# Performance work log

Measured on AMD Instinct MI355X. Metric: run time of the kernel, lower is better.

The kernel has to match this reference:

```python
import jax, jax.numpy as jnp
import numpy as np

H = 16  # num_heads (inner_dim 1024 // default head_dim 64)
D = 64  # head_dim
EPS = 1e-5

def layernorm(x, w, b):
    mu = jnp.mean(x, axis=-1, keepdims=True)
    var = jnp.var(x, axis=-1, keepdims=True)
    return (x - mu) * jax.lax.rsqrt(var + EPS) * w + b

def attention(x, kv, wq, wk, wv, wo, bo):
    b, t, c = x.shape
    s = kv.shape[1]
    q = (x @ wq).reshape(b, t, H, D).transpose(0, 2, 1, 3)   # bhtd
    k = (kv @ wk).reshape(b, s, H, D).transpose(0, 2, 1, 3)  # bhsd
    v = (kv @ wv).reshape(b, s, H, D).transpose(0, 2, 1, 3)
    scores = jnp.einsum('bhqd,bhkd->bhqk', q, k) * (D ** -0.5)
    attn = jax.nn.softmax(scores, axis=-1)
    out = jnp.einsum('bhqk,bhkd->bhqd', attn, v)
    out = out.transpose(0, 2, 1, 3).reshape(b, t, c)
    return out @ wo + bo

def setup_inputs() -> dict:
    key = jax.random.key(0)
    ks = jax.random.split(key, 16)
    hs = 1024
    dff = 4 * hs  # 4096
    sc = lambda fan_in: 1.0 / np.sqrt(fan_in)
    inp = {
        'x': jax.random.normal(ks[0], (2, 2048, hs), jnp.float32),
        'encoder_hidden_states': jax.random.normal(ks[1], (2, 512, 64), jnp.float32),
        'ln1_w': jnp.ones((hs,), jnp.float32), 'ln1_b': jnp.zeros((hs,), jnp.float32),
        'a1_wq': jax.random.normal(ks[2], (hs, hs), jnp.float32) * sc(hs),
        'a1_wk': jax.random.normal(ks[3], (hs, hs), jnp.float32) * sc(hs),
        'a1_wv': jax.random.normal(ks[4], (hs, hs), jnp.float32) * sc(hs),
        'a1_wo': jax.random.normal(ks[5], (hs, hs), jnp.float32) * sc(hs),
        'a1_bo': jnp.zeros((hs,), jnp.float32),
        'ln2_w': jnp.ones((hs,), jnp.float32), 'ln2_b': jnp.zeros((hs,), jnp.float32),
        'a2_wq': jax.random.normal(ks[6], (hs, hs), jnp.float32) * sc(hs),
        'a2_wk': jax.random.normal(ks[7], (64, hs), jnp.float32) * sc(64),
        'a2_wv': jax.random.normal(ks[8], (64, hs), jnp.float32) * sc(64),
        'a2_wo': jax.random.normal(ks[9], (hs, hs), jnp.float32) * sc(hs),
        'a2_bo': jnp.zeros((hs,), jnp.float32),
        'ln3_w': jnp.ones((hs,), jnp.float32), 'ln3_b': jnp.zeros((hs,), jnp.float32),
        'ff_w1': jax.random.normal(ks[10], (hs, 2 * dff), jnp.float32) * sc(hs),
        'ff_b1': jnp.zeros((2 * dff,), jnp.float32),
        'ff_w2': jax.random.normal(ks[11], (dff, hs), jnp.float32) * sc(dff),
        'ff_b2': jnp.zeros((hs,), jnp.float32),
    }
    return inp

def reference(x, encoder_hidden_states, ln1_w, ln1_b, a1_wq, a1_wk, a1_wv, a1_wo, a1_bo,
              ln2_w, ln2_b, a2_wq, a2_wk, a2_wv, a2_wo, a2_bo,
              ln3_w, ln3_b, ff_w1, ff_b1, ff_w2, ff_b2):
    # self-attention sub-block
    h = layernorm(x, ln1_w, ln1_b)
    x = x + attention(h, h, a1_wq, a1_wk, a1_wv, a1_wo, a1_bo)
    # cross-attention sub-block (kv from encoder_hidden_states, dim 64)
    h = layernorm(x, ln2_w, ln2_b)
    x = x + attention(h, encoder_hidden_states, a2_wq, a2_wk, a2_wv, a2_wo, a2_bo)
    # GEGLU feed-forward sub-block
    h = layernorm(x, ln3_w, ln3_b)
    hp = h @ ff_w1 + ff_b1
    h1, h2 = jnp.split(hp, 2, axis=-1)
    h = (h1 * jax.nn.gelu(h2, approximate=False)) @ ff_w2 + ff_b2
    return x + h
```

## Files before the change

### kernel.cpp

```cpp
#include <hip/hip_runtime.h>
#include <hip/hip_bf16.h>
#include <stdint.h>

typedef unsigned short u16;
typedef __bf16 bf16x8 __attribute__((ext_vector_type(8)));
typedef float f32x4 __attribute__((ext_vector_type(4)));
typedef u16 u16x8 __attribute__((ext_vector_type(8)));
typedef u16 u16x4 __attribute__((ext_vector_type(4)));

__device__ __forceinline__ u16 f2bf(float f) {
  union { float f; uint32_t u; } v; v.f = f;
  uint32_t r = v.u + 0x7fffu + ((v.u >> 16) & 1u);
  return (u16)(r >> 16);
}
__device__ __forceinline__ float bf2f(u16 u) {
  union { uint32_t u; float f; } v; v.u = ((uint32_t)u) << 16;
  return v.f;
}
__device__ __forceinline__ uint32_t cvtpk(float a, float b) {
  uint32_t r;
  asm("v_cvt_pk_bf16_f32 %0, %1, %2" : "=v"(r) : "v"(a), "v"(b));
  return r;
}

__device__ __forceinline__ void gld16(const u16* g, u16* l) {
  __builtin_amdgcn_global_load_lds(
      (const __attribute__((address_space(1))) uint32_t*)g,
      (__attribute__((address_space(3))) uint32_t*)l, 16, 0, 0);
}

__device__ __forceinline__ void stage_half(const u16* __restrict__ gbase, int ldg,
                                           u16* lbase, int tid) {
#pragma unroll
  for (int j = 0; j < 2; ++j) {
    const int idx = j * 512 + tid;
    const int row = idx >> 3, c8 = idx & 7;
    gld16(gbase + (size_t)row * ldg + ((c8 ^ (row & 7)) << 3), lbase + idx * 8);
  }
}

struct WB {
  const float* src[6];
  u16* dst[6];
  float scale[6];
};
__global__ void wconv_b(WB wb, int K, int N) {
  const int z = blockIdx.z;
  const float* __restrict__ W = wb.src[z];
  u16* __restrict__ Wt = wb.dst[z];
  const float scale = wb.scale[z];
  __shared__ float tile[32][33];
  const int n0 = blockIdx.x * 32, k0 = blockIdx.y * 32;
  const int tx = threadIdx.x, ty = threadIdx.y;
#pragma unroll
  for (int i = 0; i < 4; ++i)
    tile[ty + 8 * i][tx] = W[(size_t)(k0 + ty + 8 * i) * N + n0 + tx];
  __syncthreads();
#pragma unroll
  for (int i = 0; i < 4; ++i)
    Wt[(size_t)(n0 + ty + 8 * i) * K + k0 + tx] = f2bf(scale * tile[tx][ty + 8 * i]);
}

__global__ void wconv_t(const float* __restrict__ W, u16* __restrict__ Wt, int K, int N) {
  __shared__ float tile[32][33];
  const int n0 = blockIdx.x * 32, k0 = blockIdx.y * 32;
  const int tx = threadIdx.x, ty = threadIdx.y;
#pragma unroll
  for (int i = 0; i < 4; ++i)
    tile[ty + 8 * i][tx] = W[(size_t)(k0 + ty + 8 * i) * N + n0 + tx];
  __syncthreads();
#pragma unroll
  for (int i = 0; i < 4; ++i)
    Wt[(size_t)(n0 + ty + 8 * i) * K + k0 + tx] = f2bf(tile[tx][ty + 8 * i]);
}

__global__ void wconv_g(const float* __restrict__ W, u16* __restrict__ Wt) {
  __shared__ float tile[32][33];
  const int n0 = blockIdx.x * 32, k0 = blockIdx.y * 32;
  const int tx = threadIdx.x, ty = threadIdx.y;
#pragma unroll
  for (int i = 0; i < 4; ++i)
    tile[ty + 8 * i][tx] = W[(size_t)(k0 + ty + 8 * i) * 8192 + n0 + tx];
  __syncthreads();
#pragma unroll
  for (int i = 0; i < 4; ++i) {
    const int n = n0 + ty + 8 * i;
    const int p = (((n & 4095) >> 7) << 8) + (((n >> 12) & 1) << 7) + (n & 127);
    Wt[(size_t)p * 1024 + k0 + tx] = f2bf(tile[tx][ty + 8 * i]);
  }
}

__global__ void cvt_bf(const float* __restrict__ in, u16* __restrict__ out, int n) {
  int i = blockIdx.x * 256 + threadIdx.x;
  if (i < n) out[i] = f2bf(in[i]);
}

__global__ __launch_bounds__(256)
void vtrans(const u16* __restrict__ V, int ldv, int hoff, u16* __restrict__ Vt, int S) {
  __shared__ u16 tile[64][72];
  const int t0 = blockIdx.x, bh = blockIdx.y;
  const int b = bh >> 4, hc = (bh & 15) * 64 + hoff;
  const int tid = threadIdx.x;
  const int r = tid >> 2, dq = (tid & 3) * 16;
  const int pos = ((r >> 5) << 5) | (((r >> 2) & 3) << 3) | (((r >> 4) & 1) << 2) | (r & 3);
  const size_t grow = ((size_t)b * S + t0 * 64 + r) * ldv + hc + dq;
  u16x8 v1 = *(const u16x8*)&V[grow];
  u16x8 v2 = *(const u16x8*)&V[grow + 8];
#pragma unroll
  for (int j = 0; j < 8; ++j) {
    tile[dq + j][pos] = v1[j];
    tile[dq + 8 + j][pos] = v2[j];
  }
  __syncthreads();
  const int d = tid >> 2, c = (tid & 3) * 16;
  u16x8 o1, o2;
#pragma unroll
  for (int j = 0; j < 8; ++j) { o1[j] = tile[d][c + j]; o2[j] = tile[d][c + 8 + j]; }
  *(u16x8*)&Vt[((size_t)bh * 64 + d) * S + t0 * 64 + c] = o1;
  *(u16x8*)&Vt[((size_t)bh * 64 + d) * S + t0 * 64 + c + 8] = o2;
}

__global__ __launch_bounds__(256)
void ln_fwd(const float* __restrict__ X, const float* __restrict__ wt,
            const float* __restrict__ bs, u16* __restrict__ Y) {
  const int row = blockIdx.x, t = threadIdx.x;
  const float4 v = *(const float4*)&X[(size_t)row * 1024 + t * 4];
  float s = v.x + v.y + v.z + v.w;
  float s2 = v.x * v.x + v.y * v.y + v.z * v.z + v.w * v.w;
#pragma unroll
  for (int off = 32; off > 0; off >>= 1) {
    s += __shfl_xor(s, off);
    s2 += __shfl_xor(s2, off);
  }
  __shared__ float rs[4], rs2[4];
  const int w = t >> 6;
  if ((t & 63) == 0) { rs[w] = s; rs2[w] = s2; }
  __syncthreads();
  s = rs[0] + rs[1] + rs[2] + rs[3];
  s2 = rs2[0] + rs2[1] + rs2[2] + rs2[3];
  const float mu = s * (1.0f / 1024.0f);
  const float var = s2 * (1.0f / 1024.0f) - mu * mu;
  const float rstd = rsqrtf(var + 1e-5f);
  const float4 wv = *(const float4*)&wt[t * 4];
  const float4 bv = *(const float4*)&bs[t * 4];
  u16x4 o;
  o[0] = f2bf((v.x - mu) * rstd * wv.x + bv.x);
  o[1] = f2bf((v.y - mu) * rstd * wv.y + bv.y);
  o[2] = f2bf((v.z - mu) * rstd * wv.z + bv.z);
  o[3] = f2bf((v.w - mu) * rstd * wv.w + bv.w);
  *(u16x4*)&Y[(size_t)row * 1024 + t * 4] = o;
}

template<int TN>
__global__ __launch_bounds__(256, 2)
void gemm_bf16(const u16* __restrict__ A, int lda, const u16* __restrict__ Bt,
               int M, int N, int K, const float* __restrict__ bias,
               const float* __restrict__ resid, float oscale,
               float* __restrict__ outF, u16* __restrict__ outB) {
  constexpr int WNV = (TN == 128) ? 2 : 1;
  constexpr int WMV = 4 / WNV;
  constexpr int WM = 128 / WMV;
  constexpr int WN = TN / WNV;
  constexpr int MI = WM / 16, NI = WN / 16;
  __shared__ __align__(16) u16 Al[128 * 64];
  __shared__ __align__(16) u16 Bl[TN * 64];
  const int tid = threadIdx.x;
  const int w = tid >> 6, l = tid & 63, lo = l & 15, g = l >> 4;
  const int gx = gridDim.x, nwg = gx * gridDim.y;
  const int lin = blockIdx.y * gx + blockIdx.x;
  const int q = nwg >> 3, r = nwg & 7;
  const int xcd = lin & 7, pos = lin >> 3;
  const int sid = (xcd < r ? xcd * (q + 1) : r * (q + 1) + (xcd - r) * q) + pos;
  const int bm = (sid % gx) * 128, bn = (sid / gx) * TN;
  const int wm = (w / WNV) * WM, wn = (w % WNV) * WN;
  f32x4 acc[MI][NI] = {};

  for (int k0 = 0; k0 < K; k0 += 64) {
#pragma unroll
    for (int p = 0; p < 4; ++p) {
      int idx = p * 256 + tid;
      int row = idx >> 3, c = idx & 7;
      gld16(A + (size_t)(bm + row) * lda + k0 + c * 8, &Al[idx * 8]);
    }
#pragma unroll
    for (int p = 0; p < TN / 32; ++p) {
      int idx = p * 256 + tid;
      int row = idx >> 3, c = idx & 7;
      gld16(Bt + (size_t)(bn + row) * K + k0 + c * 8, &Bl[idx * 8]);
    }
    asm volatile("s_waitcnt vmcnt(0)" ::: "memory");
    __syncthreads();
#pragma unroll
    for (int ks = 0; ks < 2; ++ks) {
      bf16x8 af[MI], bf[NI];
#pragma unroll
      for (int i = 0; i < MI; ++i)
        af[i] = *(const bf16x8*)&Al[(wm + i * 16 + lo) * 64 + ks * 32 + g * 8];
#pragma unroll
      for (int i = 0; i < NI; ++i)
        bf[i] = *(const bf16x8*)&Bl[(wn + i * 16 + lo) * 64 + ks * 32 + g * 8];
#pragma unroll
      for (int mi = 0; mi < MI; ++mi)
#pragma unroll
        for (int ni = 0; ni < NI; ++ni)
          acc[mi][ni] = __builtin_amdgcn_mfma_f32_16x16x32_bf16(af[mi], bf[ni], acc[mi][ni], 0, 0, 0);
    }
    __syncthreads();
  }

#pragma unroll
  for (int mi = 0; mi < MI; ++mi) {
#pragma unroll
    for (int ni = 0; ni < NI; ++ni) {
      const int col = bn + wn + ni * 16 + lo;
      const float bb = bias ? bias[col] : 0.0f;
      const int row0 = bm + wm + mi * 16 + g * 4;
#pragma unroll
      for (int rr = 0; rr < 4; ++rr) {
        const size_t off = (size_t)(row0 + rr) * N + col;
        float v = acc[mi][ni][rr] * oscale + bb;
        if (resid) v += resid[off];
        if (outF) outF[off] = v;
        else outB[off] = f2bf(v);
      }
    }
  }
}

template<int MODE>
__global__ __launch_bounds__(512, 2)
void gemm256(const u16* __restrict__ A, int lda, const u16* __restrict__ Bt,
             int M, int N, int K, const float* __restrict__ bias,
             const float* __restrict__ resid, float oscale,
             float* __restrict__ outF, u16* __restrict__ outB) {
  __shared__ __align__(16) u16 sm[65536];
  const int tid = threadIdx.x;
  const int w = tid >> 6, l = tid & 63, lo = l & 15, g = l >> 4;
  const int wrow = w >> 2, wcol = w & 3;
  const int gx = gridDim.x;
  const int nwg = gx * gridDim.y;
  const int lin = blockIdx.y * gx + blockIdx.x;
  const int q = nwg >> 3, r = nwg & 7;
  const int xcd = lin & 7, pos = lin >> 3;
  const int sid = (xcd < r ? xcd * (q + 1) : r * (q + 1) + (xcd - r) * q) + pos;
  const int bm = (sid % gx) * 256, bn = (sid / gx) * 256;

  const int NT = K >> 6;
  const int swz = (lo & 7) << 3;
  f32x4 acc[8][4] = {};

  stage_half(Bt + (size_t)bn * K, K, sm + 16384, tid);
  stage_half(Bt + (size_t)(bn + 128) * K, K, sm + 16384 + 8192, tid);
  stage_half(A + (size_t)bm * lda, lda, sm, tid);
  stage_half(A + (size_t)(bm + 128) * lda, lda, sm + 8192, tid);
  if (NT > 1) {
    stage_half(Bt + (size_t)bn * K + 64, K, sm + 32768 + 16384, tid);
    stage_half(Bt + (size_t)(bn + 128) * K + 64, K, sm + 32768 + 16384 + 8192, tid);
    stage_half(A + (size_t)bm * lda + 64, lda, sm + 32768, tid);
  }
  asm volatile("s_waitcnt vmcnt(6)" ::: "memory");
  __builtin_amdgcn_s_barrier();

  for (int t = 0; t < NT; ++t) {
    u16* Ab_ = sm + (t & 1) * 32768;
    u16* Bb_ = Ab_ + 16384;
    bf16x8 a0[4][2], a1[4][2], b01[2][2], b23[2][2];
#pragma unroll
    for (int mf = 0; mf < 4; ++mf) {
      const int rowi = wrow * 128 + mf * 16 + lo;
#pragma unroll
      for (int kk = 0; kk < 2; ++kk)
        a0[mf][kk] = *(const bf16x8*)&Ab_[rowi * 64 + ((kk * 32 + g * 8) ^ swz)];
    }
#pragma unroll
    for (int nf = 0; nf < 2; ++nf) {
      const int rowi = wcol * 64 + nf * 16 + lo;
#pragma unroll
      for (int kk = 0; kk < 2; ++kk)
        b01[nf][kk] = *(const bf16x8*)&Bb_[rowi * 64 + ((kk * 32 + g * 8) ^ swz)];
    }
    __builtin_amdgcn_sched_barrier(0);
#pragma unroll
    for (int nf = 0; nf < 2; ++nf) {
      const int rowi = wcol * 64 + 32 + nf * 16 + lo;
#pragma unroll
      for (int kk = 0; kk < 2; ++kk)
        b23[nf][kk] = *(const bf16x8*)&Bb_[rowi * 64 + ((kk * 32 + g * 8) ^ swz)];
    }
    __builtin_amdgcn_sched_barrier(0);
    if (t + 1 < NT)
      stage_half(A + (size_t)(bm + 128) * lda + (t + 1) * 64, lda,
                 sm + ((t + 1) & 1) * 32768 + 8192, tid);
    __builtin_amdgcn_s_barrier();
    asm volatile("s_waitcnt lgkmcnt(4)" ::: "memory");
    __builtin_amdgcn_sched_barrier(0);
    __builtin_amdgcn_s_setprio(1);
#pragma unroll
    for (int mf = 0; mf < 4; ++mf)
#pragma unroll
      for (int nf = 0; nf < 2; ++nf)
#pragma unroll
        for (int kk = 0; kk < 2; ++kk)
          acc[mf][nf] = __builtin_amdgcn_mfma_f32_16x16x32_bf16(a0[mf][kk], b01[nf][kk], acc[mf][nf], 0, 0, 0);
    __builtin_amdgcn_s_setprio(0);
    __builtin_amdgcn_s_barrier();
#pragma unroll
    for (int mf = 0; mf < 4; ++mf) {
      const int rowi = wrow * 128 + 64 + mf * 16 + lo;
#pragma unroll
      for (int kk = 0; kk < 2; ++kk)
        a1[mf][kk] = *(const bf16x8*)&Ab_[rowi * 64 + ((kk * 32 + g * 8) ^ swz)];
    }
    __builtin_amdgcn_sched_barrier(0);
    if (t + 2 < NT)
      stage_half(Bt + (size_t)bn * K + (t + 2) * 64, K,
                 sm + (t & 1) * 32768 + 16384, tid);
    __builtin_amdgcn_s_barrier();
    asm volatile("s_waitcnt lgkmcnt(8)" ::: "memory");
    __builtin_amdgcn_sched_barrier(0);
    __builtin_amdgcn_s_setprio(1);
#pragma unroll
    for (int mf = 0; mf < 4; ++mf)
#pragma unroll
      for (int nf = 0; nf < 2; ++nf)
#pragma unroll
        for (int kk = 0; kk < 2; ++kk)
          acc[mf][2 + nf] = __builtin_amdgcn_mfma_f32_16x16x32_bf16(a0[mf][kk], b23[nf][kk], acc[mf][2 + nf], 0, 0, 0);
    __builtin_amdgcn_s_setprio(0);
    __builtin_amdgcn_s_barrier();
    if (t + 2 < NT)
      stage_half(Bt + (size_t)(bn + 128) * K + (t + 2) * 64, K,
                 sm + (t & 1) * 32768 + 16384 + 8192, tid);
    __builtin_amdgcn_s_barrier();
    asm volatile("s_waitcnt lgkmcnt(0)" ::: "memory");
    __builtin_amdgcn_sched_barrier(0);
    __builtin_amdgcn_s_setprio(1);
#pragma unroll
    for (int mf = 0; mf < 4; ++mf)
#pragma unroll
      for (int nf = 0; nf < 2; ++nf)
#pragma unroll
        for (int kk = 0; kk < 2; ++kk)
          acc[4 + mf][nf] = __builtin_amdgcn_mfma_f32_16x16x32_bf16(a1[mf][kk], b01[nf][kk], acc[4 + mf][nf], 0, 0, 0);
    __builtin_amdgcn_s_setprio(0);
    __builtin_amdgcn_s_barrier();
    if (t + 2 < NT)
      stage_half(A + (size_t)bm * lda + (t + 2) * 64, lda,
                 sm + (t & 1) * 32768, tid);
    __builtin_amdgcn_s_barrier();
    __builtin_amdgcn_s_setprio(1);
#pragma unroll
    for (int mf = 0; mf < 4; ++mf)
#pragma unroll
      for (int nf = 0; nf < 2; ++nf)
#pragma unroll
        for (int kk = 0; kk < 2; ++kk)
          acc[4 + mf][2 + nf] = __builtin_amdgcn_mfma_f32_16x16x32_bf16(a1[mf][kk], b23[nf][kk], acc[4 + mf][2 + nf], 0, 0, 0);
    __builtin_amdgcn_s_setprio(0);
    if (t + 2 < NT) asm volatile("s_waitcnt vmcnt(6)" ::: "memory");
    else            asm volatile("s_waitcnt vmcnt(0)" ::: "memory");
    __builtin_amdgcn_s_barrier();
  }

  if (MODE == 1) {
    float* smf = (float*)sm;
    const int obase = bn >> 1;
    if (wcol >= 2) {
#pragma unroll
      for (int mi = 0; mi < 8; ++mi)
#pragma unroll
        for (int ni = 0; ni < 4; ++ni) {
          const int lc = (wcol - 2) * 64 + ni * 16 + lo;
          const float bb = bias[4096 + obase + lc];
#pragma unroll
          for (int rr = 0; rr < 4; ++rr) {
            const int rowi = wrow * 128 + mi * 16 + g * 4 + rr;
            const float h2 = acc[mi][ni][rr] + bb;
            smf[rowi * 128 + lc] = 0.5f * h2 * (1.0f + erff(h2 * 0.70710678118f));
          }
        }
    }
    __syncthreads();
    if (wcol < 2) {
#pragma unroll
      for (int mi = 0; mi < 8; ++mi)
#pragma unroll
        for (int ni = 0; ni < 4; ++ni) {
          const int lc = wcol * 64 + ni * 16 + lo;
          const float bb = bias[obase + lc];
#pragma unroll
          for (int rr = 0; rr < 4; ++rr) {
            const int rowi = wrow * 128 + mi * 16 + g * 4 + rr;
            const float h1 = acc[mi][ni][rr] + bb;
            outB[(size_t)(bm + rowi) * 4096 + obase + lc] = f2bf(h1 * smf[rowi * 128 + lc]);
          }
        }
    }
    return;
  }

#pragma unroll
  for (int mi = 0; mi < 8; ++mi) {
#pragma unroll
    for (int ni = 0; ni < 4; ++ni) {
      const int col = bn + wcol * 64 + ni * 16 + lo;
      const float bb = bias ? bias[col] : 0.0f;
      const int row0 = bm + wrow * 128 + mi * 16 + g * 4;
#pragma unroll
      for (int rr = 0; rr < 4; ++rr) {
        const size_t off = (size_t)(row0 + rr) * N + col;
        float v = acc[mi][ni][rr] * oscale + bb;
        if (resid) v += resid[off];
        if (outF) outF[off] = v;
        else outB[off] = f2bf(v);
      }
    }
  }
}

__global__ __launch_bounds__(256, 4)
void attn_fwd(const u16* __restrict__ Q, int ldq, const u16* __restrict__ K, int ldk,
              const u16* __restrict__ Vt, u16* __restrict__ O, int T, int S) {
  __shared__ __align__(16) u16 Kl[2][4096];
  __shared__ __align__(16) u16 Vl[2][4096];
  const int tid = threadIdx.x, w = tid >> 6, l = tid & 63, lo = l & 15, g = l >> 4;
  const int nwg = gridDim.x * gridDim.y;
  const int n = blockIdx.y * gridDim.x + blockIdx.x;
  const int sid = (n & 7) * (nwg >> 3) + (n >> 3);
  const int qt = sid % gridDim.x, bh = sid / gridDim.x;
  const int b = bh >> 4, h = bh & 15, hc = h * 64;
  const int q0 = qt * 64 + w * 16;
  const size_t qrow = (size_t)b * T + q0;
  const size_t krow0 = (size_t)b * S;
  const size_t vrow0 = (size_t)bh * 64;

  bf16x8 qf[2];
#pragma unroll
  for (int kk = 0; kk < 2; ++kk)
    qf[kk] = *(const bf16x8*)&Q[(qrow + lo) * ldq + hc + kk * 32 + g * 8];

  f32x4 oa[4] = {};
  float m = -1e30f, lsum = 0.0f;

  const int srow = tid >> 3;
  const int scol = (((tid & 7) ^ (srow & 7)) << 3);

  const int ntile = S >> 6;
#pragma unroll
  for (int c = 0; c < 2; ++c)
    gld16(K + (krow0 + c * 32 + srow) * ldk + hc + scol, &Kl[0][c * 2048 + tid * 8]);
#pragma unroll
  for (int c = 0; c < 2; ++c)
    gld16(Vt + (vrow0 + c * 32 + srow) * S + scol, &Vl[0][c * 2048 + tid * 8]);

  for (int t0 = 0; t0 < ntile; ++t0) {
    const int cur = t0 & 1;
    if (t0 + 1 < ntile) {
      const int nxt = cur ^ 1;
#pragma unroll
      for (int c = 0; c < 2; ++c)
        gld16(K + (krow0 + (t0 + 1) * 64 + c * 32 + srow) * ldk + hc + scol,
              &Kl[nxt][c * 2048 + tid * 8]);
#pragma unroll
      for (int c = 0; c < 2; ++c)
        gld16(Vt + (vrow0 + c * 32 + srow) * S + (t0 + 1) * 64 + scol,
              &Vl[nxt][c * 2048 + tid * 8]);
      asm volatile("s_waitcnt vmcnt(4)" ::: "memory");
    } else {
      asm volatile("s_waitcnt vmcnt(0)" ::: "memory");
    }
    __builtin_amdgcn_s_barrier();

    f32x4 s[4] = {};
#pragma unroll
    for (int c = 0; c < 4; ++c)
#pragma unroll
      for (int kk = 0; kk < 2; ++kk) {
        bf16x8 kf = *(const bf16x8*)&Kl[cur][(c * 16 + lo) * 64 +
                                            ((kk * 32 + g * 8) ^ ((lo & 7) << 3))];
        s[c] = __builtin_amdgcn_mfma_f32_16x16x32_bf16(kf, qf[kk], s[c], 0, 0, 0);
      }

    float mx = fmaxf(fmaxf(fmaxf(s[0][0], s[0][1]), fmaxf(s[0][2], s[0][3])),
                     fmaxf(fmaxf(s[1][0], s[1][1]), fmaxf(s[1][2], s[1][3])));
    mx = fmaxf(mx, fmaxf(fmaxf(fmaxf(s[2][0], s[2][1]), fmaxf(s[2][2], s[2][3])),
                         fmaxf(fmaxf(s[3][0], s[3][1]), fmaxf(s[3][2], s[3][3]))));
    mx = fmaxf(mx, __shfl_xor(mx, 16));
    mx = fmaxf(mx, __shfl_xor(mx, 32));
    const float mn = fmaxf(m, mx);
    const float al = exp2f(m - mn);
    m = mn;
    float psum = 0.0f;
#pragma unroll
    for (int c = 0; c < 4; ++c)
#pragma unroll
      for (int rr = 0; rr < 4; ++rr) {
        s[c][rr] = exp2f(s[c][rr] - mn);
        psum += s[c][rr];
      }
    psum += __shfl_xor(psum, 16);
    psum += __shfl_xor(psum, 32);
    lsum = lsum * al + psum;
    f32x4 arv;
#pragma unroll
    for (int rr = 0; rr < 4; ++rr) arv[rr] = __shfl(al, 20 * g + rr);
#pragma unroll
    for (int dn = 0; dn < 4; ++dn) oa[dn] *= arv;

    union { uint32_t u[4]; bf16x8 v; } af[2];
#pragma unroll
    for (int ks = 0; ks < 2; ++ks) {
      af[ks].u[0] = cvtpk(s[2 * ks][0], s[2 * ks][1]);
      af[ks].u[1] = cvtpk(s[2 * ks][2], s[2 * ks][3]);
      af[ks].u[2] = cvtpk(s[2 * ks + 1][0], s[2 * ks + 1][1]);
      af[ks].u[3] = cvtpk(s[2 * ks + 1][2], s[2 * ks + 1][3]);
    }
#pragma unroll
    for (int dn = 0; dn < 4; ++dn)
#pragma unroll
      for (int ks = 0; ks < 2; ++ks) {
        bf16x8 vf = *(const bf16x8*)&Vl[cur][(dn * 16 + lo) * 64 +
                                            ((ks * 32 + g * 8) ^ ((lo & 7) << 3))];
        oa[dn] = __builtin_amdgcn_mfma_f32_16x16x32_bf16(af[ks].v, vf, oa[dn], 0, 0, 0);
      }
    asm volatile("s_waitcnt lgkmcnt(0)" ::: "memory");
    __builtin_amdgcn_s_barrier();
  }

  const float il = 1.0f / lsum;
  float ir[4];
#pragma unroll
  for (int rr = 0; rr < 4; ++rr) ir[rr] = __shfl(il, 20 * g + rr);
#pragma unroll
  for (int dn = 0; dn < 4; ++dn)
#pragma unroll
    for (int rr = 0; rr < 4; ++rr)
      O[(qrow + g * 4 + rr) * 1024 + hc + dn * 16 + lo] = f2bf(oa[dn][rr] * ir[rr]);
}

extern "C" void kernel_launch(void* const* d_in, const int* in_sizes, int n_in,
                              void* d_out, int out_size, void* d_ws, size_t ws_size,
                              hipStream_t stream) {
  const float* x      = (const float*)d_in[0];
  const float* enc    = (const float*)d_in[1];
  const float* ln1_w  = (const float*)d_in[2];
  const float* ln1_b  = (const float*)d_in[3];
  const float* a1_wq  = (const float*)d_in[4];
  const float* a1_wk  = (const float*)d_in[5];
  const float* a1_wv  = (const float*)d_in[6];
  const float* a1_wo  = (const float*)d_in[7];
  const float* a1_bo  = (const float*)d_in[8];
  const float* ln2_w  = (const float*)d_in[9];
  const float* ln2_b  = (const float*)d_in[10];
  const float* a2_wq  = (const float*)d_in[11];
  const float* a2_wk  = (const float*)d_in[12];
  const float* a2_wv  = (const float*)d_in[13];
  const float* a2_wo  = (const float*)d_in[14];
  const float* a2_bo  = (const float*)d_in[15];
  const float* ln3_w  = (const float*)d_in[16];
  const float* ln3_b  = (const float*)d_in[17];
  const float* ff_w1  = (const float*)d_in[18];
  const float* ff_b1  = (const float*)d_in[19];
  const float* ff_w2  = (const float*)d_in[20];
  const float* ff_b2  = (const float*)d_in[21];

  char* ws = (char*)d_ws;
  const size_t MB = 1u << 20;
  u16* wqkv1t = (u16*)(ws + 0 * MB);
  u16* wo1t   = (u16*)(ws + 6 * MB);
  u16* wq2t   = (u16*)(ws + 8 * MB);
  u16* wo2t   = (u16*)(ws + 10 * MB);
  u16* wkv2t  = (u16*)(ws + 12 * MB);
  u16* encb   = (u16*)(ws + 12 * MB + 512 * 1024);
  u16* w1t    = (u16*)(ws + 13 * MB);
  u16* w2t    = (u16*)(ws + 29 * MB);
  float* x2   = (float*)(ws + 37 * MB);
  u16* Vt1    = (u16*)(ws + 37 * MB);
  u16* Vt2    = (u16*)(ws + 45 * MB);
  u16* KVb    = (u16*)(ws + 47 * MB);
  u16* hbuf   = (u16*)(ws + 53 * MB);
  u16* qkv    = (u16*)(ws + 61 * MB);
  u16* Qb     = (u16*)(ws + 61 * MB);
  u16* Ab     = (u16*)(ws + 85 * MB);
  float* x1   = (float*)(ws + 93 * MB);
  u16* gq     = (u16*)(ws + 61 * MB);

  const float SCL = 0.125f * 1.44269504f;
  const dim3 tb(32, 8);
  {
    WB wb;
    wb.src[0] = a1_wq; wb.dst[0] = wqkv1t;               wb.scale[0] = SCL;
    wb.src[1] = a1_wk; wb.dst[1] = wqkv1t + 1024 * 1024; wb.scale[1] = 1.0f;
    wb.src[2] = a1_wv; wb.dst[2] = wqkv1t + 2048 * 1024; wb.scale[2] = 1.0f;
    wb.src[3] = a1_wo; wb.dst[3] = wo1t;                 wb.scale[3] = 1.0f;
    wb.src[4] = a2_wq; wb.dst[4] = wq2t;                 wb.scale[4] = SCL;
    wb.src[5] = a2_wo; wb.dst[5] = wo2t;                 wb.scale[5] = 1.0f;
    wconv_b<<<dim3(32, 32, 6), tb, 0, stream>>>(wb, 1024, 1024);
    WB wb2;
    wb2.src[0] = a2_wk; wb2.dst[0] = wkv2t;             wb2.scale[0] = 1.0f;
    wb2.src[1] = a2_wv; wb2.dst[1] = wkv2t + 64 * 1024; wb2.scale[1] = 1.0f;
    wb2.src[2] = a2_wk; wb2.dst[2] = wkv2t;             wb2.scale[2] = 1.0f;
    wb2.src[3] = a2_wk; wb2.dst[3] = wkv2t;             wb2.scale[3] = 1.0f;
    wb2.src[4] = a2_wk; wb2.dst[4] = wkv2t;             wb2.scale[4] = 1.0f;
    wb2.src[5] = a2_wk; wb2.dst[5] = wkv2t;             wb2.scale[5] = 1.0f;
    wconv_b<<<dim3(32, 2, 2), tb, 0, stream>>>(wb2, 64, 1024);
  }
  wconv_g<<<dim3(256, 32), tb, 0, stream>>>(ff_w1, w1t);
  wconv_t<<<dim3(32, 128), tb, 0, stream>>>(ff_w2, w2t, 4096, 1024);
  cvt_bf<<<256, 256, 0, stream>>>(enc, encb, 2 * 512 * 64);

  ln_fwd<<<4096, 256, 0, stream>>>(x, ln1_w, ln1_b, hbuf);
  gemm256<0><<<dim3(16, 12), 512, 0, stream>>>(hbuf, 1024, wqkv1t, 4096, 3072, 1024, nullptr, nullptr, 1.0f, nullptr, qkv);
  vtrans<<<dim3(32, 32), 256, 0, stream>>>(qkv, 3072, 2048, Vt1, 2048);
  attn_fwd<<<dim3(32, 32), 256, 0, stream>>>(qkv, 3072, qkv + 1024, 3072, Vt1, Ab, 2048, 2048);
  gemm_bf16<64><<<dim3(32, 16), 256, 0, stream>>>(Ab, 1024, wo1t, 4096, 1024, 1024, a1_bo, x, 1.0f, x1, nullptr);

  ln_fwd<<<4096, 256, 0, stream>>>(x1, ln2_w, ln2_b, hbuf);
  gemm_bf16<64><<<dim3(32, 16), 256, 0, stream>>>(hbuf, 1024, wq2t, 4096, 1024, 1024, nullptr, nullptr, 1.0f, nullptr, Qb);
  gemm_bf16<64><<<dim3(8, 32), 256, 0, stream>>>(encb, 64, wkv2t, 1024, 2048, 64, nullptr, nullptr, 1.0f, nullptr, KVb);
  vtrans<<<dim3(8, 32), 256, 0, stream>>>(KVb + 1024, 2048, 0, Vt2, 512);
  attn_fwd<<<dim3(32, 32), 256, 0, stream>>>(Qb, 1024, KVb, 2048, Vt2, Ab, 2048, 512);
  gemm_bf16<64><<<dim3(32, 16), 256, 0, stream>>>(Ab, 1024, wo2t, 4096, 1024, 1024, a2_bo, x1, 1.0f, x2, nullptr);

  ln_fwd<<<4096, 256, 0, stream>>>(x2, ln3_w, ln3_b, hbuf);
  gemm256<1><<<dim3(16, 32), 512, 0, stream>>>(hbuf, 1024, w1t, 4096, 8192, 1024, ff_b1, nullptr, 1.0f, nullptr, gq);
  gemm_bf16<64><<<dim3(32, 16), 256, 0, stream>>>(gq, 4096, w2t, 4096, 1024, 4096, ff_b2, x2, 1.0f, (float*)d_out, nullptr);
}
```

Measured before the change: 468.7 us.

## Reorder GEMM main-loop LDS fragment loads and swizzle GEGLU epilogue smem

Merges the two B-fragment loads into one batch issued up front with a full lgkmcnt(0) wait, and moves the a1 fragment loads to after the second MFMA block. Several sched_barriers and partial lgkmcnt waits are removed, so the compiler has more freedom to schedule. The GEGLU epilogue's shared-memory staging gets an XOR swizzle on the column index to reduce bank conflicts. The risk is less overlap of LDS reads with MFMA work, because the first compute block now waits for all fragment loads to finish.

```diff
diff --git a/kernel.cpp b/kernel.cpp
--- a/kernel.cpp
+++ b/kernel.cpp
@@ -264,7 +264,7 @@
   for (int t = 0; t < NT; ++t) {
     u16* Ab_ = sm + (t & 1) * 32768;
     u16* Bb_ = Ab_ + 16384;
-    bf16x8 a0[4][2], a1[4][2], b01[2][2], b23[2][2];
+    bf16x8 a0[4][2], a1[4][2], bfr[4][2];
 #pragma unroll
     for (int mf = 0; mf < 4; ++mf) {
       const int rowi = wrow * 128 + mf * 16 + lo;
@@ -273,27 +273,17 @@
         a0[mf][kk] = *(const bf16x8*)&Ab_[rowi * 64 + ((kk * 32 + g * 8) ^ swz)];
     }
 #pragma unroll
-    for (int nf = 0; nf < 2; ++nf) {
+    for (int nf = 0; nf < 4; ++nf) {
       const int rowi = wcol * 64 + nf * 16 + lo;
 #pragma unroll
       for (int kk = 0; kk < 2; ++kk)
-        b01[nf][kk] = *(const bf16x8*)&Bb_[rowi * 64 + ((kk * 32 + g * 8) ^ swz)];
-    }
-    __builtin_amdgcn_sched_barrier(0);
-#pragma unroll
-    for (int nf = 0; nf < 2; ++nf) {
-      const int rowi = wcol * 64 + 32 + nf * 16 + lo;
-#pragma unroll
-      for (int kk = 0; kk < 2; ++kk)
-        b23[nf][kk] = *(const bf16x8*)&Bb_[rowi * 64 + ((kk * 32 + g * 8) ^ swz)];
-    }
-    __builtin_amdgcn_sched_barrier(0);
+        bfr[nf][kk] = *(const bf16x8*)&Bb_[rowi * 64 + ((kk * 32 + g * 8) ^ swz)];
+    }
     if (t + 1 < NT)
       stage_half(A + (size_t)(bm + 128) * lda + (t + 1) * 64, lda,
                  sm + ((t + 1) & 1) * 32768 + 8192, tid);
     __builtin_amdgcn_s_barrier();
-    asm volatile("s_waitcnt lgkmcnt(4)" ::: "memory");
-    __builtin_amdgcn_sched_barrier(0);
+    asm volatile("s_waitcnt lgkmcnt(0)" ::: "memory");
     __builtin_amdgcn_s_setprio(1);
 #pragma unroll
     for (int mf = 0; mf < 4; ++mf)
@@ -301,39 +291,35 @@
       for (int nf = 0; nf < 2; ++nf)
 #pragma unroll
         for (int kk = 0; kk < 2; ++kk)
-          acc[mf][nf] = __builtin_amdgcn_mfma_f32_16x16x32_bf16(a0[mf][kk], b01[nf][kk], acc[mf][nf], 0, 0, 0);
+          acc[mf][nf] = __builtin_amdgcn_mfma_f32_16x16x32_bf16(a0[mf][kk], bfr[nf][kk], acc[mf][nf], 0, 0, 0);
     __builtin_amdgcn_s_setprio(0);
     __builtin_amdgcn_s_barrier();
-#pragma unroll
-    for (int mf = 0; mf < 4; ++mf) {
-      const int rowi = wrow * 128 + 64 + mf * 16 + lo;
-#pragma unroll
-      for (int kk = 0; kk < 2; ++kk)
-        a1[mf][kk] = *(const bf16x8*)&Ab_[rowi * 64 + ((kk * 32 + g * 8) ^ swz)];
-    }
-    __builtin_amdgcn_sched_barrier(0);
     if (t + 2 < NT)
       stage_half(Bt + (size_t)bn * K + (t + 2) * 64, K,
                  sm + (t & 1) * 32768 + 16384, tid);
     __builtin_amdgcn_s_barrier();
-    asm volatile("s_waitcnt lgkmcnt(8)" ::: "memory");
-    __builtin_amdgcn_sched_barrier(0);
     __builtin_amdgcn_s_setprio(1);
 #pragma unroll
     for (int mf = 0; mf < 4; ++mf)
 #pragma unroll
-      for (int nf = 0; nf < 2; ++nf)
+      for (int nf = 2; nf < 4; ++nf)
 #pragma unroll
         for (int kk = 0; kk < 2; ++kk)
-          acc[mf][2 + nf] = __builtin_amdgcn_mfma_f32_16x16x32_bf16(a0[mf][kk], b23[nf][kk], acc[mf][2 + nf], 0, 0, 0);
+          acc[mf][nf] = __builtin_amdgcn_mfma_f32_16x16x32_bf16(a0[mf][kk], bfr[nf][kk], acc[mf][nf], 0, 0, 0);
     __builtin_amdgcn_s_setprio(0);
     __builtin_amdgcn_s_barrier();
+#pragma unroll
+    for (int mf = 0; mf < 4; ++mf) {
+      const int rowi = wrow * 128 + 64 + mf * 16 + lo;
+#pragma unroll
+      for (int kk = 0; kk < 2; ++kk)
+        a1[mf][kk] = *(const bf16x8*)&Ab_[rowi * 64 + ((kk * 32 + g * 8) ^ swz)];
+    }
     if (t + 2 < NT)
       stage_half(Bt + (size_t)(bn + 128) * K + (t + 2) * 64, K,
                  sm + (t & 1) * 32768 + 16384 + 8192, tid);
     __builtin_amdgcn_s_barrier();
     asm volatile("s_waitcnt lgkmcnt(0)" ::: "memory");
-    __builtin_amdgcn_sched_barrier(0);
     __builtin_amdgcn_s_setprio(1);
 #pragma unroll
     for (int mf = 0; mf < 4; ++mf)
@@ -341,7 +327,7 @@
       for (int nf = 0; nf < 2; ++nf)
 #pragma unroll
         for (int kk = 0; kk < 2; ++kk)
-          acc[4 + mf][nf] = __builtin_amdgcn_mfma_f32_16x16x32_bf16(a1[mf][kk], b01[nf][kk], acc[4 + mf][nf], 0, 0, 0);
+          acc[4 + mf][nf] = __builtin_amdgcn_mfma_f32_16x16x32_bf16(a1[mf][kk], bfr[nf][kk], acc[4 + mf][nf], 0, 0, 0);
     __builtin_amdgcn_s_setprio(0);
     __builtin_amdgcn_s_barrier();
     if (t + 2 < NT)
@@ -352,10 +338,10 @@
 #pragma unroll
     for (int mf = 0; mf < 4; ++mf)
 #pragma unroll
-      for (int nf = 0; nf < 2; ++nf)
+      for (int nf = 2; nf < 4; ++nf)
 #pragma unroll
         for (int kk = 0; kk < 2; ++kk)
-          acc[4 + mf][2 + nf] = __builtin_amdgcn_mfma_f32_16x16x32_bf16(a1[mf][kk], b23[nf][kk], acc[4 + mf][2 + nf], 0, 0, 0);
+          acc[4 + mf][nf] = __builtin_amdgcn_mfma_f32_16x16x32_bf16(a1[mf][kk], bfr[nf][kk], acc[4 + mf][nf], 0, 0, 0);
     __builtin_amdgcn_s_setprio(0);
     if (t + 2 < NT) asm volatile("s_waitcnt vmcnt(6)" ::: "memory");
     else            asm volatile("s_waitcnt vmcnt(0)" ::: "memory");
@@ -376,7 +362,8 @@
           for (int rr = 0; rr < 4; ++rr) {
             const int rowi = wrow * 128 + mi * 16 + g * 4 + rr;
             const float h2 = acc[mi][ni][rr] + bb;
-            smf[rowi * 128 + lc] = 0.5f * h2 * (1.0f + erff(h2 * 0.70710678118f));
+            smf[rowi * 128 + (lc ^ ((rowi & 12) << 1))] =
+                0.5f * h2 * (1.0f + erff(h2 * 0.70710678118f));
           }
         }
     }
@@ -392,7 +379,8 @@
           for (int rr = 0; rr < 4; ++rr) {
             const int rowi = wrow * 128 + mi * 16 + g * 4 + rr;
             const float h1 = acc[mi][ni][rr] + bb;
-            outB[(size_t)(bm + rowi) * 4096 + obase + lc] = f2bf(h1 * smf[rowi * 128 + lc]);
+            outB[(size_t)(bm + rowi) * 4096 + obase + lc] =
+                f2bf(h1 * smf[rowi * 128 + (lc ^ ((rowi & 12) << 1))]);
           }
         }
     }
```

Measured after the change: 469.4 us. About the same (+0.1%).
